# Kernel optimization log

Measured on AMD Instinct MI355X. Metric: run time of the kernel, lower is better.

## Reference

```python
import jax, jax.numpy as jnp
import numpy as np

NEG_SLOPE = 0.2  # LeakyReLU(0.2)
DN = ('NCDHW', 'OIDHW', 'NCDHW')


def leaky(x):
    return jnp.where(x >= 0, x, NEG_SLOPE * x)


def conv3d(x, w, stride=1, pad=1):
    return jax.lax.conv_general_dilated(
        x, w, (stride,) * 3, [(pad, pad)] * 3, dimension_numbers=DN)


def down_mask(m):
    # active output sites of a k=3, s=2, p=1 sparse conv = maxpool of input mask
    return jax.lax.reduce_window(
        m, 0.0, jax.lax.max, (1, 1, 3, 3, 3), (1, 1, 2, 2, 2),
        [(0, 0), (0, 0), (1, 1), (1, 1), (1, 1)])


def res_block(x, m, wa, wb, wdn):
    # SubMConv3d == dense conv masked to active sites (inactive inputs are zero)
    identity = conv3d(x, wdn, 1, 0) * m if wdn is not None else x
    out = leaky(conv3d(x, wa) * m)
    out = conv3d(out, wb) * m
    return leaky(out + identity)


def setup_inputs() -> dict:
    key = jax.random.key(0)
    ks = jax.random.split(key, 12)
    B, D = 2, 64
    occ = jax.random.uniform(ks[0], (B, 1, D, D, D)) < 0.05
    mask = occ.astype(jnp.float32)
    x = jax.random.normal(ks[1], (B, 3, D, D, D), jnp.float32) * mask

    def w(k, o, i, ksz):
        fan = i * ksz ** 3
        return jax.random.normal(k, (o, i, ksz, ksz, ksz), jnp.float32) / np.sqrt(fan).astype(np.float32)

    return {
        'x': x, 'mask': mask,
        # stage1 (in 3 -> 64), has 1x1 downsample
        'w1a': w(ks[2], 64, 3, 3), 'w1b': w(ks[3], 64, 64, 3), 'w1d': w(ks[4], 64, 3, 1),
        'wd1': w(ks[5], 128, 64, 3),   # down1 stride 2
        'w2a': w(ks[6], 128, 128, 3), 'w2b': w(ks[7], 128, 128, 3),  # stage2
        'wd2': w(ks[8], 256, 128, 3),  # down2 stride 2
        'w3a': w(ks[9], 256, 256, 3), 'w3b': w(ks[10], 256, 256, 3),  # stage3
        'wd3': w(ks[11], 128, 256, 3),  # down3 stride 2 -> out_ch=128
    }


def reference(x, mask, w1a, w1b, w1d, wd1, w2a, w2b, wd2, w3a, w3b, wd3):
    m1 = mask
    m2 = down_mask(m1)
    m3 = down_mask(m2)

    x1 = res_block(x, m1, w1a, w1b, w1d)          # [B,64,64,64,64]
    x = leaky(conv3d(x1, wd1, stride=2))           # [B,128,32,32,32]
    x2 = res_block(x, m2, w2a, w2b, None)
    x = leaky(conv3d(x2, wd2, stride=2))           # [B,256,16,16,16]
    x3 = res_block(x, m3, w3a, w3b, None)
    x4 = leaky(conv3d(x3, wd3, stride=2))          # [B,128,8,8,8] == x4.dense()

    avg = x4.mean(axis=(2, 3, 4))
    mx = x4.max(axis=(2, 3, 4))
    return jnp.concatenate([avg, mx], axis=1)      # [B,256]
```

## Files before the change

### kernel.cpp

```cpp
#include <hip/hip_runtime.h>


enum { EPI_MASK = 1, EPI_LEAKY = 2, EPI_RESID = 4 };
#define ROWCAP 32768

typedef short  bf16x8 __attribute__((ext_vector_type(8)));
typedef float  f32x4  __attribute__((ext_vector_type(4)));
typedef ushort us4    __attribute__((ext_vector_type(4)));

__device__ __forceinline__ float leaky(float v) { return v >= 0.f ? v : 0.2f * v; }
__device__ __forceinline__ ushort f2bf(float f) {
    unsigned u = __float_as_uint(f);
    return (ushort)((u + 0x7FFFu + ((u >> 16) & 1u)) >> 16);
}
__device__ __forceinline__ float bf2f(ushort h) {
    return __uint_as_float((unsigned)h << 16);
}
__device__ __forceinline__ int choff(int c) {
    return (c >> 5) * 64 + ((c >> 3) & 3) * 16 + (c & 7);
}

__global__ __launch_bounds__(256) void transpose_w_kernel(
    const float* __restrict__ w, float* __restrict__ wT, int CO, int CIK)
{
    int i = blockIdx.x * 256 + threadIdx.x;
    if (i >= CO * CIK) return;
    int co = i / CIK, r = i - co * CIK;
    wT[(size_t)r * CO + co] = w[i];
}

__global__ __launch_bounds__(256) void pack_w1b_kernel(
    const float* __restrict__ w, float* __restrict__ wT)
{
    int i = blockIdx.x * 256 + threadIdx.x;
    if (i >= 27 * 64 * 64) return;
    int co = i & 63, ci = (i >> 6) & 63, t = i >> 12;
    wT[i] = w[(co * 64 + ci) * 27 + t];
}

__global__ __launch_bounds__(256) void pack_wd1_kernel(
    const float* __restrict__ w, float* __restrict__ wP)
{
    int i = blockIdx.x * 256 + threadIdx.x;
    if (i >= 27 * 64 * 128) return;
    int co = i & 127, ci = (i >> 7) & 63, t = i >> 13;
    wP[i] = w[(co * 64 + ci) * 27 + t];
}

__global__ __launch_bounds__(256) void pack_w_kernel(
    const float* __restrict__ w, ushort* __restrict__ A, int CI, int CO)
{
    int i = blockIdx.x * 256 + threadIdx.x;
    if (i >= 27 * CI * CO * 2) return;
    int j = i & 7, hilo = (i >> 3) & 1, L = (i >> 4) & 63, rest = i >> 10;
    int NMT = CO >> 4, NCI = CI >> 5;
    int mt = rest % NMT; rest /= NMT;
    int ct = rest % NCI;
    int tap = rest / NCI;
    int co = mt * 16 + (L & 15);
    int ci = ct * 32 + (L >> 4) * 8 + j;
    float v = w[((size_t)co * CI + ci) * 27 + tap];
    ushort h = f2bf(v);
    A[i] = hilo ? f2bf(v - bf2f(h)) : h;
}

template<int DIN, int DOUT>
__global__ __launch_bounds__(256) void maxpool_kernel(
    const float* __restrict__ in, float* __restrict__ out)
{
    int i = blockIdx.x * 256 + threadIdx.x;
    constexpr int D3O = DOUT * DOUT * DOUT;
    if (i >= 2 * D3O) return;
    int b = i / D3O;
    int v = i - b * D3O;
    int z = v / (DOUT * DOUT), y = (v / DOUT) % DOUT, x = v % DOUT;
    float mx = 0.f;
    #pragma unroll
    for (int dz = 0; dz < 3; ++dz)
        #pragma unroll
        for (int dy = 0; dy < 3; ++dy)
            #pragma unroll
            for (int dx = 0; dx < 3; ++dx) {
                int zi = 2 * z - 1 + dz, yi = 2 * y - 1 + dy, xi = 2 * x - 1 + dx;
                if ((unsigned)zi < (unsigned)DIN && (unsigned)yi < (unsigned)DIN &&
                    (unsigned)xi < (unsigned)DIN)
                    mx = fmaxf(mx, in[(size_t)b * DIN * DIN * DIN + (zi * DIN + yi) * DIN + xi]);
            }
    out[i] = mx;
}

__global__ __launch_bounds__(256) void build_list_kernel(
    const float* __restrict__ m, int* __restrict__ list, int* __restrict__ idxmap,
    int* __restrict__ count)
{
    int i = blockIdx.x * 256 + threadIdx.x;
    if (i >= 2 * 262144) return;
    if (m[i] > 0.5f) {
        int k = atomicAdd(count, 1);
        if (k < ROWCAP) {
            list[k] = i;
            idxmap[i] = k;
        }
    }
}

__global__ __launch_bounds__(64) void stage1a_kernel(
    const float* __restrict__ x, const float* __restrict__ waT,
    const int* __restrict__ list, const int* __restrict__ count,
    float* __restrict__ t1c)
{
    __shared__ float smem[81];
    int n = min(*count, ROWCAP);
    for (int i = blockIdx.x; i < n; i += gridDim.x) {
        int lin = list[i];
        int b = lin >> 18;
        int v = lin & 262143;
        int z = v >> 12, y = (v >> 6) & 63, xx = v & 63;
        for (int j = threadIdx.x; j < 81; j += 64) {
            int ci = j / 27, t = j - ci * 27;
            int zz = z + t / 9 - 1, yy = y + (t / 3) % 3 - 1, xc = xx + t % 3 - 1;
            float val = 0.f;
            if ((unsigned)zz < 64u && (unsigned)yy < 64u && (unsigned)xc < 64u)
                val = x[(size_t)(b * 3 + ci) * 262144 + (zz << 12) + (yy << 6) + xc];
            smem[j] = val;
        }
        __syncthreads();
        float acc = 0.f;
        #pragma unroll 9
        for (int j = 0; j < 81; ++j)
            acc = fmaf(smem[j], waT[j * 64 + threadIdx.x], acc);
        t1c[(size_t)i * 64 + threadIdx.x] = leaky(acc);
        __syncthreads();
    }
}

__global__ __launch_bounds__(64) void stage1b_kernel(
    const float* __restrict__ t1c, const float* __restrict__ x,
    const float* __restrict__ w1bT,
    const float* __restrict__ wdT,
    const int* __restrict__ list, const int* __restrict__ idxmap,
    const int* __restrict__ count,
    float* __restrict__ x1c)
{
    __shared__ int   srr[27];
    __shared__ float sx[27][64];
    int n = min(*count, ROWCAP);
    int i = blockIdx.x;
    if (i >= n) return;
    const int tid = threadIdx.x;
    int lin = list[i];
    int b = lin >> 18;
    int v = lin & 262143;
    int z = v >> 12, y = (v >> 6) & 63, xx = v & 63;
    const int* im = idxmap + b * 262144;

    if (tid < 27) {
        int kz = tid / 9, ky = (tid / 3) % 3, kx = tid % 3;
        int zz = z + kz - 1, yy = y + ky - 1, xc = xx + kx - 1;
        int r = -1;
        if ((unsigned)zz < 64u && (unsigned)yy < 64u && (unsigned)xc < 64u)
            r = im[(zz << 12) + (yy << 6) + xc];
        srr[tid] = r;
    }
    __syncthreads();
    #pragma unroll 1
    for (int t = 0; t < 27; ++t) {
        int r = srr[t];
        if (r >= 0)
            sx[t][tid] = t1c[(size_t)r * 64 + tid];
    }
    __syncthreads();

    float acc = 0.f;
    #pragma unroll 1
    for (int t = 0; t < 27; ++t) {
        if (srr[t] < 0) continue;
        const float* wp = w1bT + (size_t)t * 4096 + tid;
        const float* xr = sx[t];
        #pragma unroll 8
        for (int ci = 0; ci < 64; ++ci)
            acc = fmaf(xr[ci], wp[ci * 64], acc);
    }
    float id = 0.f;
    #pragma unroll
    for (int ci = 0; ci < 3; ++ci)
        id = fmaf(x[(size_t)(b * 3 + ci) * 262144 + v], wdT[ci * 64 + tid], id);
    x1c[(size_t)i * 64 + tid] = leaky(acc + id);
}

__global__ __launch_bounds__(128) void wd1_kernel(
    const float* __restrict__ x1c, const int* __restrict__ idxmap,
    const float* __restrict__ wP,
    ushort* __restrict__ outp)
{
    __shared__ int   srr[27];
    __shared__ float sx[27][64];
    const int tid = threadIdx.x;
    const int v = blockIdx.x;
    const int b = blockIdx.y;
    const int zo = v >> 10, yo = (v >> 5) & 31, xo = v & 31;
    const int* im = idxmap + b * 262144;

    if (tid < 27) {
        int kz = tid / 9, ky = (tid / 3) % 3, kx = tid % 3;
        int zi = 2 * zo - 1 + kz, yi = 2 * yo - 1 + ky, xi = 2 * xo - 1 + kx;
        int r = -1;
        if ((unsigned)zi < 64u && (unsigned)yi < 64u && (unsigned)xi < 64u)
            r = im[(zi << 12) + (yi << 6) + xi];
        srr[tid] = r;
    }
    __syncthreads();
    #pragma unroll 1
    for (int t = 0; t < 27; ++t) {
        int r = srr[t];
        if (r >= 0 && tid < 64)
            sx[t][tid] = x1c[(size_t)r * 64 + tid];
    }
    __syncthreads();

    float acc = 0.f;
    #pragma unroll 1
    for (int t = 0; t < 27; ++t) {
        if (srr[t] < 0) continue;
        const float* wp = wP + (size_t)t * 8192 + tid;
        const float* xr = sx[t];
        #pragma unroll 8
        for (int ci = 0; ci < 64; ++ci)
            acc = fmaf(xr[ci], wp[ci * 128], acc);
    }
    float val = leaky(acc);
    ushort hb = f2bf(val);
    ushort lb = f2bf(val - bf2f(hb));
    size_t vb = ((((size_t)b * 32 + zo) * 32 + yo) * 33 + xo) * 256 + 256;
    int off = choff(tid);
    outp[vb + off] = hb;
    outp[vb + off + 8] = lb;
}

template<int CI, int CO, int DI, int DO, int STRIDE, int RY, int NX, int NCT, int WPEU, int EPI>
__global__ __launch_bounds__(256, WPEU) void mfma_conv6_kernel(
    const ushort* __restrict__ inp, const ushort* __restrict__ A,
    const float* __restrict__ mask, const ushort* __restrict__ resid,
    ushort* __restrict__ outp)
{
    constexpr int NCI = CI / 32;
    constexpr int NMT = CO / 16;
    constexpr int CV = CI * 2;
    constexpr int CVO = CO * 2;
    constexpr int YG = DO / RY;
    constexpr int NXV = (DO - 1) * STRIDE + 3;
    constexpr int LVS = (STRIDE == 2) ? 68 : 72;
    constexpr int NGRP = RY * NXV * 8;

    __shared__ ushort sB[RY * NXV * LVS];

    const int rg = (blockIdx.x & 7) * ((int)gridDim.x >> 3) + (blockIdx.x >> 3);
    const int y0 = (rg % YG) * RY;
    const int z = (rg / YG) % DO;
    const int b = rg / (YG * DO);
    const int wave = threadIdx.x >> 6;
    const int lane = threadIdx.x & 63;
    const int n_l = lane & 15;
    const int q = lane >> 4;
    const int mt0 = (blockIdx.y * 4 + wave) * NCT;

    f32x4 acc[NCT][RY][NX];
    #pragma unroll
    for (int a = 0; a < NCT; ++a)
        #pragma unroll
        for (int r = 0; r < RY; ++r)
            #pragma unroll
            for (int c = 0; c < NX; ++c)
                acc[a][r][c] = (f32x4){0.f, 0.f, 0.f, 0.f};

    #pragma unroll 1
    for (int ct = 0; ct < NCI; ++ct) {
        #pragma unroll 1
        for (int dz = 0; dz < 3; ++dz) {
            int zp = z * STRIDE + dz - 1;
            bool vz = (unsigned)zp < (unsigned)DI;
            int zpc = vz ? zp : 0;
            #pragma unroll 1
            for (int dy = 0; dy < 3; ++dy) {
                long rowb[RY];
                #pragma unroll
                for (int ry = 0; ry < RY; ++ry) {
                    int yp = (y0 + ry) * STRIDE + dy - 1;
                    bool v = vz && ((unsigned)yp < (unsigned)DI);
                    rowb[ry] = v ? (((((long)b * DI + zpc) * DI + yp) * (DI + 1)) * CV + CV) : -1;
                }
                __syncthreads();
                for (int g = threadIdx.x; g < NGRP; g += 256) {
                    int r = g / (NXV * 8);
                    int rem = g - r * (NXV * 8);
                    int xv = rem >> 3;
                    int gg = rem & 7;
                    long src = (rowb[r] >= 0)
                             ? (rowb[r] + (long)(xv - 1) * CV + ct * 64 + gg * 8)
                             : (long)(ct * 64 + gg * 8);
                    *(bf16x8*)(sB + (r * NXV + xv) * LVS + gg * 8) = *(const bf16x8*)(inp + src);
                }
                __syncthreads();
                #pragma unroll
                for (int dx = 0; dx < 3; ++dx) {
                    const int tap = dz * 9 + dy * 3 + dx;
                    bf16x8 bh[RY][NX], bl[RY][NX];
                    #pragma unroll
                    for (int ry = 0; ry < RY; ++ry)
                        #pragma unroll
                        for (int nx = 0; nx < NX; ++nx) {
                            int xv = (nx * 16 + n_l) * STRIDE + dx;
                            const ushort* p = sB + (ry * NXV + xv) * LVS + q * 16;
                            bh[ry][nx] = *(const bf16x8*)p;
                            bl[ry][nx] = *(const bf16x8*)(p + 8);
                        }
                    bf16x8 ahf[NCT], alf[NCT];
                    #pragma unroll
                    for (int mt = 0; mt < NCT; ++mt) {
                        size_t aa = ((size_t)(tap * NCI + ct) * NMT + (mt0 + mt)) * 1024 + lane * 16;
                        ahf[mt] = *(const bf16x8*)(A + aa);
                        alf[mt] = *(const bf16x8*)(A + aa + 8);
                    }
                    #pragma unroll
                    for (int mt = 0; mt < NCT; ++mt)
                        #pragma unroll
                        for (int ry = 0; ry < RY; ++ry)
                            #pragma unroll
                            for (int nx = 0; nx < NX; ++nx)
                                acc[mt][ry][nx] = __builtin_amdgcn_mfma_f32_16x16x32_bf16(ahf[mt], bh[ry][nx], acc[mt][ry][nx], 0, 0, 0);
                    #pragma unroll
                    for (int mt = 0; mt < NCT; ++mt)
                        #pragma unroll
                        for (int ry = 0; ry < RY; ++ry)
                            #pragma unroll
                            for (int nx = 0; nx < NX; ++nx)
                                acc[mt][ry][nx] = __builtin_amdgcn_mfma_f32_16x16x32_bf16(ahf[mt], bl[ry][nx], acc[mt][ry][nx], 0, 0, 0);
                    #pragma unroll
                    for (int mt = 0; mt < NCT; ++mt)
                        #pragma unroll
                        for (int ry = 0; ry < RY; ++ry)
                            #pragma unroll
                            for (int nx = 0; nx < NX; ++nx)
                                acc[mt][ry][nx] = __builtin_amdgcn_mfma_f32_16x16x32_bf16(alf[mt], bh[ry][nx], acc[mt][ry][nx], 0, 0, 0);
                }
            }
        }
    }

    #pragma unroll
    for (int ry = 0; ry < RY; ++ry) {
        int yo = y0 + ry;
        #pragma unroll
        for (int nx = 0; nx < NX; ++nx) {
            int xo = nx * 16 + n_l;
            size_t vb = ((((size_t)b * DO + z) * DO + yo) * (DO + 1)) * CVO + CVO + (size_t)xo * CVO;
            float mval = 1.f;
            if (EPI & EPI_MASK) mval = mask[(((size_t)b * DO + z) * DO + yo) * DO + xo];
            #pragma unroll
            for (int mt = 0; mt < NCT; ++mt) {
                int c0 = (mt0 + mt) * 16 + q * 4;
                size_t oa = vb + choff(c0);
                float rs[4] = {0.f, 0.f, 0.f, 0.f};
                if (EPI & EPI_RESID) {
                    us4 rh4 = *(const us4*)(resid + oa);
                    us4 rl4 = *(const us4*)(resid + oa + 8);
                    #pragma unroll
                    for (int r = 0; r < 4; ++r) rs[r] = bf2f(rh4[r]) + bf2f(rl4[r]);
                }
                us4 oh, ol;
                #pragma unroll
                for (int r = 0; r < 4; ++r) {
                    float v = acc[mt][ry][nx][r];
                    if (EPI & EPI_MASK) v *= mval;
                    if (EPI & EPI_RESID) v += rs[r];
                    if (EPI & EPI_LEAKY) v = leaky(v);
                    ushort hb = f2bf(v);
                    oh[r] = hb;
                    ol[r] = f2bf(v - bf2f(hb));
                }
                *(us4*)(outp + oa) = oh;
                *(us4*)(outp + oa + 8) = ol;
            }
        }
    }
}

template<int CI, int CO, int DI, int RY, int NX, int NCT, int WPEU, int EPI>
__global__ __launch_bounds__(256, WPEU) void mfma_conv8_kernel(
    const ushort* __restrict__ inp, const ushort* __restrict__ A,
    const float* __restrict__ mask, const ushort* __restrict__ resid,
    ushort* __restrict__ outp)
{
    constexpr int DO = DI;
    constexpr int NCI = CI / 32;
    constexpr int NMT = CO / 16;
    constexpr int CV = CI * 2;
    constexpr int CVO = CO * 2;
    constexpr int YG = DO / RY;
    constexpr int NYR = RY + 2;
    constexpr int NXV = DO + 2;
    constexpr int LVS = 72;
    constexpr int NGRP = NYR * NXV * 8;

    __shared__ ushort sB[NYR * NXV * LVS];

    const int rg = (blockIdx.x & 7) * ((int)gridDim.x >> 3) + (blockIdx.x >> 3);
    const int y0 = (rg % YG) * RY;
    const int z = (rg / YG) % DO;
    const int b = rg / (YG * DO);
    const int wave = threadIdx.x >> 6;
    const int lane = threadIdx.x & 63;
    const int n_l = lane & 15;
    const int q = lane >> 4;
    const int mt0 = (blockIdx.y * 4 + wave) * NCT;

    f32x4 acc[NCT][RY][NX];
    #pragma unroll
    for (int a = 0; a < NCT; ++a)
        #pragma unroll
        for (int r = 0; r < RY; ++r)
            #pragma unroll
            for (int c = 0; c < NX; ++c)
                acc[a][r][c] = (f32x4){0.f, 0.f, 0.f, 0.f};

    #pragma unroll 1
    for (int ct = 0; ct < NCI; ++ct) {
        #pragma unroll 1
        for (int dz = 0; dz < 3; ++dz) {
            int zp = z + dz - 1;
            bool vz = (unsigned)zp < (unsigned)DI;
            int zpc = vz ? zp : 0;
            __syncthreads();
            for (int g = threadIdx.x; g < NGRP; g += 256) {
                int r = g / (NXV * 8);
                int rem = g - r * (NXV * 8);
                int xv = rem >> 3;
                int gg = rem & 7;
                int yp = y0 + r - 1;
                bool v = vz & ((unsigned)yp < (unsigned)DI);
                long src = v ? ((((((long)b * DI + zpc) * DI + yp) * (DI + 1)) * CV + CV)
                                + (long)(xv - 1) * CV + ct * 64 + gg * 8)
                             : (long)(ct * 64 + gg * 8);
                *(bf16x8*)(sB + (r * NXV + xv) * LVS + gg * 8) = *(const bf16x8*)(inp + src);
            }
            __syncthreads();
            #pragma unroll 1
            for (int dy = 0; dy < 3; ++dy) {
                #pragma unroll
                for (int dx = 0; dx < 3; ++dx) {
                    const int tap = dz * 9 + dy * 3 + dx;
                    bf16x8 bh[RY][NX], bl[RY][NX];
                    #pragma unroll
                    for (int ry = 0; ry < RY; ++ry)
                        #pragma unroll
                        for (int nx = 0; nx < NX; ++nx) {
                            int xv = nx * 16 + n_l + dx;
                            const ushort* p = sB + ((ry + dy) * NXV + xv) * LVS + q * 16;
                            bh[ry][nx] = *(const bf16x8*)p;
                            bl[ry][nx] = *(const bf16x8*)(p + 8);
                        }
                    bf16x8 ahf[NCT], alf[NCT];
                    #pragma unroll
                    for (int mt = 0; mt < NCT; ++mt) {
                        size_t aa = ((size_t)(tap * NCI + ct) * NMT + (mt0 + mt)) * 1024 + lane * 16;
                        ahf[mt] = *(const bf16x8*)(A + aa);
                        alf[mt] = *(const bf16x8*)(A + aa + 8);
                    }
                    #pragma unroll
                    for (int mt = 0; mt < NCT; ++mt)
                        #pragma unroll
                        for (int ry = 0; ry < RY; ++ry)
                            #pragma unroll
                            for (int nx = 0; nx < NX; ++nx)
                                acc[mt][ry][nx] = __builtin_amdgcn_mfma_f32_16x16x32_bf16(ahf[mt], bh[ry][nx], acc[mt][ry][nx], 0, 0, 0);
                    #pragma unroll
                    for (int mt = 0; mt < NCT; ++mt)
                        #pragma unroll
                        for (int ry = 0; ry < RY; ++ry)
                            #pragma unroll
                            for (int nx = 0; nx < NX; ++nx)
                                acc[mt][ry][nx] = __builtin_amdgcn_mfma_f32_16x16x32_bf16(ahf[mt], bl[ry][nx], acc[mt][ry][nx], 0, 0, 0);
                    #pragma unroll
                    for (int mt = 0; mt < NCT; ++mt)
                        #pragma unroll
                        for (int ry = 0; ry < RY; ++ry)
                            #pragma unroll
                            for (int nx = 0; nx < NX; ++nx)
                                acc[mt][ry][nx] = __builtin_amdgcn_mfma_f32_16x16x32_bf16(alf[mt], bh[ry][nx], acc[mt][ry][nx], 0, 0, 0);
                }
            }
        }
    }

    #pragma unroll
    for (int ry = 0; ry < RY; ++ry) {
        int yo = y0 + ry;
        #pragma unroll
        for (int nx = 0; nx < NX; ++nx) {
            int xo = nx * 16 + n_l;
            size_t vb = ((((size_t)b * DO + z) * DO + yo) * (DO + 1)) * CVO + CVO + (size_t)xo * CVO;
            float mval = 1.f;
            if (EPI & EPI_MASK) mval = mask[(((size_t)b * DO + z) * DO + yo) * DO + xo];
            #pragma unroll
            for (int mt = 0; mt < NCT; ++mt) {
                int c0 = (mt0 + mt) * 16 + q * 4;
                size_t oa = vb + choff(c0);
                float rs[4] = {0.f, 0.f, 0.f, 0.f};
                if (EPI & EPI_RESID) {
                    us4 rh4 = *(const us4*)(resid + oa);
                    us4 rl4 = *(const us4*)(resid + oa + 8);
                    #pragma unroll
                    for (int r = 0; r < 4; ++r) rs[r] = bf2f(rh4[r]) + bf2f(rl4[r]);
                }
                us4 oh, ol;
                #pragma unroll
                for (int r = 0; r < 4; ++r) {
                    float v = acc[mt][ry][nx][r];
                    if (EPI & EPI_MASK) v *= mval;
                    if (EPI & EPI_RESID) v += rs[r];
                    if (EPI & EPI_LEAKY) v = leaky(v);
                    ushort hb = f2bf(v);
                    oh[r] = hb;
                    ol[r] = f2bf(v - bf2f(hb));
                }
                *(us4*)(outp + oa) = oh;
                *(us4*)(outp + oa + 8) = ol;
            }
        }
    }
}

template<int CI, int CO, int DI, int RY, int NCT, int KS, int WPEU>
__global__ __launch_bounds__(256, WPEU) void mfma_conv7_kernel(
    const ushort* __restrict__ inp, const ushort* __restrict__ A,
    float* __restrict__ part)
{
    constexpr int DO = DI;
    constexpr int NCI = CI / 32;
    constexpr int KCI = NCI / KS;
    constexpr int NMT = CO / 16;
    constexpr int CV = CI * 2;
    constexpr int YG = DO / RY;
    constexpr int NYR = RY + 2;
    constexpr int NXV = DO + 2;
    constexpr int LVS = 72;
    constexpr int NCOG = NMT / (4 * NCT);
    constexpr int D3 = DO * DO * DO;

    __shared__ ushort sB[3 * NYR * NXV * LVS];

    const int rg = (blockIdx.x & 7) * ((int)gridDim.x >> 3) + (blockIdx.x >> 3);
    const int y0 = (rg % YG) * RY;
    const int z = (rg / YG) % DO;
    const int b = rg / (YG * DO);
    const int wave = threadIdx.x >> 6;
    const int lane = threadIdx.x & 63;
    const int n_l = lane & 15;
    const int q = lane >> 4;
    const int cog = blockIdx.y % NCOG;
    const int kc = blockIdx.y / NCOG;
    const int mt0 = (cog * 4 + wave) * NCT;

    f32x4 acc[NCT][RY];
    #pragma unroll
    for (int a = 0; a < NCT; ++a)
        #pragma unroll
        for (int r = 0; r < RY; ++r)
            acc[a][r] = (f32x4){0.f, 0.f, 0.f, 0.f};

    #pragma unroll 1
    for (int ctl = 0; ctl < KCI; ++ctl) {
        const int ct = kc * KCI + ctl;
        __syncthreads();
        for (int g = threadIdx.x; g < 3 * NYR * NXV * 8; g += 256) {
            int row = g / (NXV * 8);
            int rem = g - row * (NXV * 8);
            int xv = rem >> 3;
            int gg = rem & 7;
            int zi = row / NYR, yr = row - zi * NYR;
            int zp = z + zi - 1;
            int yp = y0 + yr - 1;
            bool v = ((unsigned)zp < (unsigned)DI) & ((unsigned)yp < (unsigned)DI);
            long src = v ? ((((((long)b * DI + zp) * DI + yp) * (DI + 1)) * CV + CV)
                            + (long)(xv - 1) * CV + ct * 64 + gg * 8)
                         : (long)(ct * 64 + gg * 8);
            *(bf16x8*)(sB + (row * NXV + xv) * LVS + gg * 8) = *(const bf16x8*)(inp + src);
        }
        __syncthreads();
        #pragma unroll 1
        for (int dz = 0; dz < 3; ++dz) {
            #pragma unroll 1
            for (int dy = 0; dy < 3; ++dy) {
                #pragma unroll
                for (int dx = 0; dx < 3; ++dx) {
                    const int tap = dz * 9 + dy * 3 + dx;
                    bf16x8 bh[RY], bl[RY];
                    #pragma unroll
                    for (int ry = 0; ry < RY; ++ry) {
                        const ushort* p = sB + ((dz * NYR + ry + dy) * NXV + n_l + dx) * LVS + q * 16;
                        bh[ry] = *(const bf16x8*)p;
                        bl[ry] = *(const bf16x8*)(p + 8);
                    }
                    bf16x8 ahf[NCT], alf[NCT];
                    #pragma unroll
                    for (int mt = 0; mt < NCT; ++mt) {
                        size_t aa = ((size_t)(tap * NCI + ct) * NMT + (mt0 + mt)) * 1024 + lane * 16;
                        ahf[mt] = *(const bf16x8*)(A + aa);
                        alf[mt] = *(const bf16x8*)(A + aa + 8);
                    }
                    #pragma unroll
                    for (int mt = 0; mt < NCT; ++mt)
                        #pragma unroll
                        for (int ry = 0; ry < RY; ++ry)
                            acc[mt][ry] = __builtin_amdgcn_mfma_f32_16x16x32_bf16(ahf[mt], bh[ry], acc[mt][ry], 0, 0, 0);
                    #pragma unroll
                    for (int mt = 0; mt < NCT; ++mt)
                        #pragma unroll
                        for (int ry = 0; ry < RY; ++ry)
                            acc[mt][ry] = __builtin_amdgcn_mfma_f32_16x16x32_bf16(ahf[mt], bl[ry], acc[mt][ry], 0, 0, 0);
                    #pragma unroll
                    for (int mt = 0; mt < NCT; ++mt)
                        #pragma unroll
                        for (int ry = 0; ry < RY; ++ry)
                            acc[mt][ry] = __builtin_amdgcn_mfma_f32_16x16x32_bf16(alf[mt], bh[ry], acc[mt][ry], 0, 0, 0);
                }
            }
        }
    }

    #pragma unroll
    for (int ry = 0; ry < RY; ++ry) {
        int yo = y0 + ry;
        int v = (z * DO + yo) * DO + n_l;
        #pragma unroll
        for (int mt = 0; mt < NCT; ++mt) {
            int c0 = (mt0 + mt) * 16 + q * 4;
            size_t off = (((size_t)kc * 2 + b) * D3 + v) * CO + c0;
            *(f32x4*)(part + off) = acc[mt][ry];
        }
    }
}

__global__ __launch_bounds__(256) void combine3_kernel(
    const float* __restrict__ part, const float* __restrict__ mask,
    const ushort* __restrict__ resid, ushort* __restrict__ outp)
{
    int i = blockIdx.x * 256 + threadIdx.x;
    if (i >= 2 * 4096 * 64) return;
    int g = i & 63, v = (i >> 6) & 4095, b = i >> 18;
    int c0 = g * 4;
    size_t p0 = (((size_t)b) * 4096 + v) * 256 + c0;
    float4 s0 = *(const float4*)(part + p0);
    float4 s1 = *(const float4*)(part + p0 + (size_t)2 * 4096 * 256);
    float m = mask[b * 4096 + v];
    int z = v >> 8, y = (v >> 4) & 15, x = v & 15;
    size_t vb = ((((size_t)b * 16 + z) * 16 + y) * 17) * 512 + 512 + (size_t)x * 512;
    size_t oa = vb + choff(c0);
    float rs[4] = {0.f, 0.f, 0.f, 0.f};
    if (resid) {
        us4 rh = *(const us4*)(resid + oa);
        us4 rl = *(const us4*)(resid + oa + 8);
        #pragma unroll
        for (int r = 0; r < 4; ++r) rs[r] = bf2f(rh[r]) + bf2f(rl[r]);
    }
    float sv[4] = {s0.x + s1.x, s0.y + s1.y, s0.z + s1.z, s0.w + s1.w};
    us4 oh, ol;
    #pragma unroll
    for (int r = 0; r < 4; ++r) {
        float val = sv[r] * m + rs[r];
        val = leaky(val);
        ushort hb = f2bf(val);
        oh[r] = hb;
        ol[r] = f2bf(val - bf2f(hb));
    }
    *(us4*)(outp + oa) = oh;
    *(us4*)(outp + oa + 8) = ol;
}

__global__ __launch_bounds__(256) void wd3_mfma_kernel(
    const ushort* __restrict__ x3, const ushort* __restrict__ A,
    float* __restrict__ x4)
{
    constexpr int NCI = 8;
    constexpr int NMT = 8;
    const int blk = blockIdx.x;
    const int yg = blk & 3;
    const int z = (blk >> 2) & 7;
    const int b = blk >> 5;
    const int wave = threadIdx.x >> 6;
    const int lane = threadIdx.x & 63;
    const int n_l = lane & 15;
    const int q = lane >> 4;
    const int y = yg * 2 + (n_l >> 3);
    const int x = n_l & 7;
    const int mt0 = wave * 2;

    f32x4 acc[2];
    acc[0] = (f32x4){0.f, 0.f, 0.f, 0.f};
    acc[1] = (f32x4){0.f, 0.f, 0.f, 0.f};
    const bf16x8 zero8 = {0, 0, 0, 0, 0, 0, 0, 0};

    for (int ct = 0; ct < NCI; ++ct) {
        #pragma unroll
        for (int dz = 0; dz < 3; ++dz) {
            int zp = 2 * z + dz - 1;
            if ((unsigned)zp >= 16u) continue;
            #pragma unroll
            for (int dy = 0; dy < 3; ++dy) {
                int yp = 2 * y + dy - 1;
                bool vy = (unsigned)yp < 16u;
                int ypc = vy ? yp : 0;
                #pragma unroll
                for (int dx = 0; dx < 3; ++dx) {
                    int xp = 2 * x + dx - 1;
                    int tap = dz * 9 + dy * 3 + dx;
                    size_t ba = ((((size_t)b * 16 + zp) * 16 + ypc) * 17 + 1 + xp) * 512
                              + ct * 64 + q * 16;
                    bf16x8 bh = vy ? *(const bf16x8*)(x3 + ba) : zero8;
                    bf16x8 bl = vy ? *(const bf16x8*)(x3 + ba + 8) : zero8;
                    bf16x8 ahf[2], alf[2];
                    #pragma unroll
                    for (int mt = 0; mt < 2; ++mt) {
                        size_t aa = ((size_t)(tap * NCI + ct) * NMT + (mt0 + mt)) * 1024 + lane * 16;
                        ahf[mt] = *(const bf16x8*)(A + aa);
                        alf[mt] = *(const bf16x8*)(A + aa + 8);
                    }
                    #pragma unroll
                    for (int mt = 0; mt < 2; ++mt)
                        acc[mt] = __builtin_amdgcn_mfma_f32_16x16x32_bf16(ahf[mt], bh, acc[mt], 0, 0, 0);
                    #pragma unroll
                    for (int mt = 0; mt < 2; ++mt)
                        acc[mt] = __builtin_amdgcn_mfma_f32_16x16x32_bf16(ahf[mt], bl, acc[mt], 0, 0, 0);
                    #pragma unroll
                    for (int mt = 0; mt < 2; ++mt)
                        acc[mt] = __builtin_amdgcn_mfma_f32_16x16x32_bf16(alf[mt], bh, acc[mt], 0, 0, 0);
                }
            }
        }
    }
    #pragma unroll
    for (int mt = 0; mt < 2; ++mt)
        #pragma unroll
        for (int r = 0; r < 4; ++r) {
            int co = (mt0 + mt) * 16 + q * 4 + r;
            x4[((size_t)(b * 128 + co)) * 512 + z * 64 + y * 8 + x] = leaky(acc[mt][r]);
        }
}

__global__ __launch_bounds__(64) void reduce_kernel(
    const float* __restrict__ x4, float* __restrict__ out)
{
    int bc = blockIdx.x;
    int b = bc >> 7, c = bc & 127;
    const float* p = x4 + (size_t)(b * 128 + c) * 512;
    float s = 0.f, mx = -3.4e38f;
    for (int i = threadIdx.x; i < 512; i += 64) {
        float v = p[i];
        s += v;
        mx = fmaxf(mx, v);
    }
    #pragma unroll
    for (int o = 32; o > 0; o >>= 1) {
        s += __shfl_down(s, o);
        mx = fmaxf(mx, __shfl_down(mx, o));
    }
    if (threadIdx.x == 0) {
        out[b * 256 + c] = s * (1.f / 512.f);
        out[b * 256 + 128 + c] = mx;
    }
}

__global__ __launch_bounds__(256) void zero_out_kernel(float* __restrict__ out, int n)
{
    int i = blockIdx.x * 256 + threadIdx.x;
    if (i < n) out[i] = 0.f;
}

extern "C" void kernel_launch(void* const* d_in, const int* in_sizes, int n_in,
                              void* d_out, int out_size, void* d_ws, size_t ws_size,
                              hipStream_t stream)
{
    (void)in_sizes; (void)n_in;
    const float* x    = (const float*)d_in[0];
    const float* mask = (const float*)d_in[1];
    const float* w1a  = (const float*)d_in[2];
    const float* w1b  = (const float*)d_in[3];
    const float* w1d  = (const float*)d_in[4];
    const float* wd1  = (const float*)d_in[5];
    const float* w2a  = (const float*)d_in[6];
    const float* w2b  = (const float*)d_in[7];
    const float* wd2  = (const float*)d_in[8];
    const float* w3a  = (const float*)d_in[9];
    const float* w3b  = (const float*)d_in[10];
    const float* wd3  = (const float*)d_in[11];
    float* out = (float*)d_out;
    char* ws = (char*)d_ws;

    const size_t RSZ = 34603520;
    const size_t SZ3 = 8913920;
    const size_t POFF = 9437184;
    char* R1 = ws;
    char* R2 = ws + RSZ;
    char* R3 = ws + 2 * RSZ;
    size_t off = 3 * RSZ;
    auto alloc = [&](size_t bytes) { char* p = ws + off; off = (off + bytes + 255) & ~255ull; return p; };
    ushort* pk2a = (ushort*)alloc(1769472);
    ushort* pk2b = (ushort*)alloc(1769472);
    ushort* pkd2 = (ushort*)alloc(3538944);
    ushort* pk3a = (ushort*)alloc(7077888);
    ushort* pk3b = (ushort*)alloc(7077888);
    float*  wd1P = (float*)alloc(884736);
    float*  waT  = (float*)alloc(20736);
    float*  w1bT = (float*)alloc(442368);
    float*  wdTt = (float*)alloc(768);
    float*  m2   = (float*)alloc(262144);
    float*  m3   = (float*)alloc(32768);
    int*    cnt  = (int*)alloc(256);
    const size_t NEED = off;

    if (ws_size < NEED) {
        zero_out_kernel<<<dim3((out_size + 255) / 256), 256, 0, stream>>>(out, out_size);
        return;
    }

    float* t1c  = (float*)R2;
    float* x1c  = (float*)(R2 + 8388608);
    int*   idx  = (int*)(R2 + 16777216);
    int*   list = (int*)(R2 + 18874368);
    ushort* pkd3 = (ushort*)R1;
    float*  x4   = (float*)R2;
    float*  part3a = (float*)(R2 + POFF);
    float*  part3b = (float*)(R3 + POFF);

    ushort* xin2 = (ushort*)R1;
    ushort* t2   = (ushort*)R2;
    ushort* x2   = (ushort*)R3;
    ushort* xin3 = (ushort*)R1;
    ushort* t3   = (ushort*)R2;
    ushort* x3   = (ushort*)R3;

    hipMemsetAsync(cnt, 0, 4, stream);
    hipMemsetAsync(idx, 0xFF, 2097152, stream);
    hipMemsetAsync(R1, 0, RSZ, stream);

    auto tg = [](int n) { return dim3((n + 255) / 256); };
    pack_w_kernel<<<tg(27 * 128 * 128 * 2), 256, 0, stream>>>(w2a, pk2a, 128, 128);
    pack_w_kernel<<<tg(27 * 128 * 128 * 2), 256, 0, stream>>>(w2b, pk2b, 128, 128);
    pack_w_kernel<<<tg(27 * 128 * 256 * 2), 256, 0, stream>>>(wd2, pkd2, 128, 256);
    pack_w_kernel<<<tg(27 * 256 * 256 * 2), 256, 0, stream>>>(w3a, pk3a, 256, 256);
    pack_w_kernel<<<tg(27 * 256 * 256 * 2), 256, 0, stream>>>(w3b, pk3b, 256, 256);
    pack_wd1_kernel    <<<tg(27 * 64 * 128), 256, 0, stream>>>(wd1, wd1P);
    transpose_w_kernel <<<tg(64 * 81),    256, 0, stream>>>(w1a, waT,  64, 81);
    pack_w1b_kernel    <<<tg(27 * 64 * 64), 256, 0, stream>>>(w1b, w1bT);
    transpose_w_kernel <<<tg(64 * 3),     256, 0, stream>>>(w1d, wdTt, 64, 3);

    maxpool_kernel<64, 32><<<dim3(2 * 32768 / 256), 256, 0, stream>>>(mask, m2);
    maxpool_kernel<32, 16><<<dim3(2 * 4096 / 256),  256, 0, stream>>>(m2, m3);
    build_list_kernel<<<dim3(2 * 262144 / 256), 256, 0, stream>>>(mask, list, idx, cnt);

    stage1a_kernel<<<dim3(2048), 64, 0, stream>>>(x, waT, list, cnt, t1c);
    stage1b_kernel<<<dim3(ROWCAP), 64, 0, stream>>>(t1c, x, w1bT, wdTt, list, idx, cnt, x1c);
    wd1_kernel<<<dim3(32768, 2), 128, 0, stream>>>(x1c, idx, wd1P, xin2);

    hipMemsetAsync(R2, 0, RSZ, stream);
    hipMemsetAsync(R3, 0, RSZ, stream);

    mfma_conv8_kernel<128, 128, 32, 2, 2, 2, 4, EPI_MASK | EPI_LEAKY>
        <<<dim3(1024, 1), 256, 0, stream>>>(xin2, pk2a, m2, nullptr, t2);
    mfma_conv8_kernel<128, 128, 32, 2, 2, 2, 4, EPI_MASK | EPI_RESID | EPI_LEAKY>
        <<<dim3(1024, 1), 256, 0, stream>>>(t2, pk2b, m2, xin2, x2);

    hipMemsetAsync(R1, 0, SZ3, stream);
    mfma_conv6_kernel<128, 256, 32, 16, 2, 2, 1, 2, 4, EPI_LEAKY>
        <<<dim3(256, 2), 256, 0, stream>>>(x2, pkd2, nullptr, nullptr, xin3);

    hipMemsetAsync(R2, 0, SZ3, stream);
    mfma_conv7_kernel<256, 256, 16, 2, 2, 2, 4>
        <<<dim3(256, 4), 256, 0, stream>>>(xin3, pk3a, part3a);
    combine3_kernel<<<dim3(2048), 256, 0, stream>>>(part3a, m3, nullptr, t3);

    hipMemsetAsync(R3, 0, SZ3, stream);
    mfma_conv7_kernel<256, 256, 16, 2, 2, 2, 4>
        <<<dim3(256, 4), 256, 0, stream>>>(t3, pk3b, part3b);
    combine3_kernel<<<dim3(2048), 256, 0, stream>>>(part3b, m3, xin3, x3);

    pack_w_kernel<<<tg(27 * 256 * 128 * 2), 256, 0, stream>>>(wd3, pkd3, 256, 128);
    wd3_mfma_kernel<<<dim3(64), 256, 0, stream>>>(x3, pkd3, x4);

    reduce_kernel<<<dim3(256), 64, 0, stream>>>(x4, out);
}
```

Before: 1.121 ms.

## Zero only padding slots instead of full buffers; iterate active taps via ballot mask

Replaces full-buffer memsets of the activation regions with a small kernel that zeroes only the x-padding slots (one per row plus a leading slot). The aim is to avoid rewriting whole multi-megabyte buffers before each conv stage. It also changes the stage1b and wd1 gather and accumulate loops to walk a ballot bitmask of active neighbour taps rather than testing all 27. The risk is correctness: this only holds if every non-padding element is overwritten by its producer kernel, including the regions that SZ3-sized buffers previously reused from earlier stages.

```diff
diff --git a/kernel.cpp b/kernel.cpp
--- a/kernel.cpp
+++ b/kernel.cpp
@@ -18,6 +18,17 @@
 }
 __device__ __forceinline__ int choff(int c) {
     return (c >> 5) * 64 + ((c >> 3) & 3) * 16 + (c & 7);
+}
+
+__global__ __launch_bounds__(256) void pad_zero_kernel(
+    ushort* __restrict__ base, int nrows, int slotstride, int slotsize)
+{
+    int i = blockIdx.x * 256 + threadIdx.x;
+    int per = slotsize >> 3;
+    int total = (nrows + 1) * per;
+    if (i >= total) return;
+    int slot = i / per, w = i - slot * per;
+    *(uint4*)(base + (size_t)slot * slotstride + w * 8) = make_uint4(0, 0, 0, 0);
 }
 
 __global__ __launch_bounds__(256) void transpose_w_kernel(
@@ -154,27 +165,29 @@
     int z = v >> 12, y = (v >> 6) & 63, xx = v & 63;
     const int* im = idxmap + b * 262144;
 
+    int r = -1;
     if (tid < 27) {
         int kz = tid / 9, ky = (tid / 3) % 3, kx = tid % 3;
         int zz = z + kz - 1, yy = y + ky - 1, xc = xx + kx - 1;
-        int r = -1;
         if ((unsigned)zz < 64u && (unsigned)yy < 64u && (unsigned)xc < 64u)
             r = im[(zz << 12) + (yy << 6) + xc];
         srr[tid] = r;
     }
+    unsigned long long mask = __ballot(r >= 0);
     __syncthreads();
-    #pragma unroll 1
-    for (int t = 0; t < 27; ++t) {
-        int r = srr[t];
-        if (r >= 0)
-            sx[t][tid] = t1c[(size_t)r * 64 + tid];
+    unsigned long long mm = mask;
+    while (mm) {
+        int t = __ffsll((unsigned long long)mm) - 1;
+        mm &= mm - 1;
+        sx[t][tid] = t1c[(size_t)srr[t] * 64 + tid];
     }
     __syncthreads();
 
     float acc = 0.f;
-    #pragma unroll 1
-    for (int t = 0; t < 27; ++t) {
-        if (srr[t] < 0) continue;
+    mm = mask;
+    while (mm) {
+        int t = __ffsll((unsigned long long)mm) - 1;
+        mm &= mm - 1;
         const float* wp = w1bT + (size_t)t * 4096 + tid;
         const float* xr = sx[t];
         #pragma unroll 8
@@ -194,6 +207,7 @@
     ushort* __restrict__ outp)
 {
     __shared__ int   srr[27];
+    __shared__ unsigned long long smask;
     __shared__ float sx[27][64];
     const int tid = threadIdx.x;
     const int v = blockIdx.x;
@@ -201,27 +215,35 @@
     const int zo = v >> 10, yo = (v >> 5) & 31, xo = v & 31;
     const int* im = idxmap + b * 262144;
 
+    int r = -1;
     if (tid < 27) {
         int kz = tid / 9, ky = (tid / 3) % 3, kx = tid % 3;
         int zi = 2 * zo - 1 + kz, yi = 2 * yo - 1 + ky, xi = 2 * xo - 1 + kx;
-        int r = -1;
         if ((unsigned)zi < 64u && (unsigned)yi < 64u && (unsigned)xi < 64u)
             r = im[(zi << 12) + (yi << 6) + xi];
         srr[tid] = r;
     }
+    if (tid < 64) {
+        unsigned long long m0 = __ballot(r >= 0);
+        if (tid == 0) smask = m0;
+    }
     __syncthreads();
-    #pragma unroll 1
-    for (int t = 0; t < 27; ++t) {
-        int r = srr[t];
-        if (r >= 0 && tid < 64)
-            sx[t][tid] = x1c[(size_t)r * 64 + tid];
+    const unsigned long long mask = smask;
+
+    unsigned long long mm = mask;
+    while (mm) {
+        int t = __ffsll((unsigned long long)mm) - 1;
+        mm &= mm - 1;
+        if (tid < 64)
+            sx[t][tid] = x1c[(size_t)srr[t] * 64 + tid];
     }
     __syncthreads();
 
     float acc = 0.f;
-    #pragma unroll 1
-    for (int t = 0; t < 27; ++t) {
-        if (srr[t] < 0) continue;
+    mm = mask;
+    while (mm) {
+        int t = __ffsll((unsigned long long)mm) - 1;
+        mm &= mm - 1;
         const float* wp = wP + (size_t)t * 8192 + tid;
         const float* xr = sx[t];
         #pragma unroll 8
@@ -839,9 +861,18 @@
     ushort* t3   = (ushort*)R2;
     ushort* x3   = (ushort*)R3;
 
+    auto pad2 = [&](void* base) {
+        pad_zero_kernel<<<dim3((2049 * 32 + 255) / 256), 256, 0, stream>>>(
+            (ushort*)base, 2048, 33 * 256, 256);
+    };
+    auto pad3 = [&](void* base) {
+        pad_zero_kernel<<<dim3((513 * 64 + 255) / 256), 256, 0, stream>>>(
+            (ushort*)base, 512, 17 * 512, 512);
+    };
+
     hipMemsetAsync(cnt, 0, 4, stream);
     hipMemsetAsync(idx, 0xFF, 2097152, stream);
-    hipMemsetAsync(R1, 0, RSZ, stream);
+    pad2(R1);
 
     auto tg = [](int n) { return dim3((n + 255) / 256); };
     pack_w_kernel<<<tg(27 * 128 * 128 * 2), 256, 0, stream>>>(w2a, pk2a, 128, 128);
@@ -862,24 +893,24 @@
     stage1b_kernel<<<dim3(ROWCAP), 64, 0, stream>>>(t1c, x, w1bT, wdTt, list, idx, cnt, x1c);
     wd1_kernel<<<dim3(32768, 2), 128, 0, stream>>>(x1c, idx, wd1P, xin2);
 
-    hipMemsetAsync(R2, 0, RSZ, stream);
-    hipMemsetAsync(R3, 0, RSZ, stream);
+    pad2(R2);
+    pad2(R3);
 
     mfma_conv8_kernel<128, 128, 32, 2, 2, 2, 4, EPI_MASK | EPI_LEAKY>
         <<<dim3(1024, 1), 256, 0, stream>>>(xin2, pk2a, m2, nullptr, t2);
     mfma_conv8_kernel<128, 128, 32, 2, 2, 2, 4, EPI_MASK | EPI_RESID | EPI_LEAKY>
         <<<dim3(1024, 1), 256, 0, stream>>>(t2, pk2b, m2, xin2, x2);
 
-    hipMemsetAsync(R1, 0, SZ3, stream);
+    pad3(R1);
     mfma_conv6_kernel<128, 256, 32, 16, 2, 2, 1, 2, 4, EPI_LEAKY>
         <<<dim3(256, 2), 256, 0, stream>>>(x2, pkd2, nullptr, nullptr, xin3);
 
-    hipMemsetAsync(R2, 0, SZ3, stream);
+    pad3(R2);
     mfma_conv7_kernel<256, 256, 16, 2, 2, 2, 4>
         <<<dim3(256, 4), 256, 0, stream>>>(xin3, pk3a, part3a);
     combine3_kernel<<<dim3(2048), 256, 0, stream>>>(part3a, m3, nullptr, t3);
 
-    hipMemsetAsync(R3, 0, SZ3, stream);
+    pad3(R3);
     mfma_conv7_kernel<256, 256, 16, 2, 2, 2, 4>
         <<<dim3(256, 4), 256, 0, stream>>>(t3, pk3b, part3b);
     combine3_kernel<<<dim3(2048), 256, 0, stream>>>(part3b, m3, xin3, x3);
```

Result: faster. 1.067 ms (-4.8%).
